# Performance work log

Measured on AMD Instinct MI355X. Metric: run time of the kernel, lower is better.

The kernel has to match this reference:

```python
import jax, jax.numpy as jnp
import numpy as np

K = 64
N = 1000000
J = 100000
B = 1048576


def setup_inputs() -> dict:
    key = jax.random.key(0)
    k1, k2, k3, k4, k5, k6, k7 = jax.random.split(key, 7)
    users = jax.random.randint(k1, (B,), 0, N, dtype=jnp.int64) if jax.config.jax_enable_x64 else jax.random.randint(k1, (B,), 0, N, dtype=jnp.int32)
    jokes = jax.random.randint(k2, (B,), 0, J, dtype=jnp.int64) if jax.config.jax_enable_x64 else jax.random.randint(k2, (B,), 0, J, dtype=jnp.int32)
    U = jax.random.normal(k3, (N, K), dtype=jnp.float32)
    V = jax.random.normal(k4, (J, K), dtype=jnp.float32)
    a = jax.random.normal(k5, (N, 1), dtype=jnp.float32)
    b = jax.random.normal(k6, (J, 1), dtype=jnp.float32)
    g = jax.random.normal(k7, (1,), dtype=jnp.float32)
    return {"users": users, "jokes": jokes, "U": U, "V": V, "a": a, "b": b, "g": g}


def reference(users, jokes, U, V, a, b, g):
    # gather latent factors and biases, fused dot + bias adds
    u = U[users]              # [B, K]
    v = V[jokes]              # [B, K]
    dot = jnp.sum(u * v, axis=-1)          # per-row dot product (bmm equivalent)
    r = dot + a[users, 0] + b[jokes, 0] + g  # broadcasts g:[1] -> [B]
    return r
```

## Files before the change

### kernel.cpp

```cpp
#include <hip/hip_runtime.h>


constexpr int KV  = 16;
constexpr int RPG = 4;

__global__ __launch_bounds__(256) void latent_linear_kernel(
    const int* __restrict__ users,
    const int* __restrict__ jokes,
    const float* __restrict__ U,
    const float* __restrict__ V,
    const float* __restrict__ a,
    const float* __restrict__ b,
    const float* __restrict__ g,
    float* __restrict__ out,
    int B)
{
    const int sub        = threadIdx.x & 15;
    const int grp_local  = threadIdx.x >> 4;
    const int grps_per_b = blockDim.x >> 4;
    const int grp_stride = gridDim.x * grps_per_b;
    const int ngroups    = B / RPG;

    const float4* __restrict__ U4 = reinterpret_cast<const float4*>(U);
    const float4* __restrict__ V4 = reinterpret_cast<const float4*>(V);
    const int4*   __restrict__ users4 = reinterpret_cast<const int4*>(users);
    const int4*   __restrict__ jokes4 = reinterpret_cast<const int4*>(jokes);

    const float g0 = g[0];

    int grp = blockIdx.x * grps_per_b + grp_local;

    if (blockIdx.x == 0 && threadIdx.x == 0) {
        for (int row = ngroups * RPG; row < B; ++row) {
            const int ui = users[row], ji = jokes[row];
            float d = 0.f;
            for (int k = 0; k < 64; ++k) d += U[(size_t)ui * 64 + k] * V[(size_t)ji * 64 + k];
            out[row] = d + a[ui] + b[ji] + g0;
        }
    }

    if (grp >= ngroups) return;

    int4 u4 = users4[grp];
    int4 j4 = jokes4[grp];

    while (grp < ngroups) {
        const int ui[RPG] = {u4.x, u4.y, u4.z, u4.w};
        const int ji[RPG] = {j4.x, j4.y, j4.z, j4.w};

        float4 uu[RPG], vv[RPG];
#pragma unroll
        for (int r = 0; r < RPG; ++r) {
            uu[r] = U4[(size_t)ui[r] * KV + sub];
            vv[r] = V4[(size_t)ji[r] * KV + sub];
        }

        float ab[RPG], bb[RPG];
#pragma unroll
        for (int r = 0; r < RPG; ++r) {
            ab[r] = a[ui[r]];
            bb[r] = b[ji[r]];
        }

        const int next = grp + grp_stride;
        if (next < ngroups) {
            u4 = users4[next];
            j4 = jokes4[next];
        }

        const int base = grp * RPG;
#pragma unroll
        for (int r = 0; r < RPG; ++r) {
            float d = uu[r].x * vv[r].x + uu[r].y * vv[r].y
                    + uu[r].z * vv[r].z + uu[r].w * vv[r].w;
            d += __shfl_down(d, 8, 16);
            d += __shfl_down(d, 4, 16);
            d += __shfl_down(d, 2, 16);
            d += __shfl_down(d, 1, 16);
            if (sub == 0)
                out[base + r] = d + ab[r] + bb[r] + g0;
        }

        grp = next;
    }
}

extern "C" void kernel_launch(void* const* d_in, const int* in_sizes, int n_in,
                              void* d_out, int out_size, void* d_ws, size_t ws_size,
                              hipStream_t stream)
{
    const int*   users = (const int*)d_in[0];
    const int*   jokes = (const int*)d_in[1];
    const float* U     = (const float*)d_in[2];
    const float* V     = (const float*)d_in[3];
    const float* a     = (const float*)d_in[4];
    const float* b     = (const float*)d_in[5];
    const float* g     = (const float*)d_in[6];
    float*       out   = (float*)d_out;

    const int B = in_sizes[0];

    const int block = 256;
    int grid = 2048;
    const int ngroups = B / RPG;
    const int max_grid = (ngroups + (block / 16) - 1) / (block / 16);
    if (grid > max_grid) grid = max_grid > 0 ? max_grid : 1;

    latent_linear_kernel<<<grid, block, 0, stream>>>(users, jokes, U, V, a, b, g, out, B);
}
```

Measured before the change: 387.3 us.

## Bucket-sort rows by user index before gathering latent factors

Adds a histogram, scan and scatter pass that bucket-sorts the batch rows by user id into 4096 buckets. The compute kernel then walks the sorted order, so U-row gathers become roughly monotone and more cache/DRAM-page friendly, and it scatters results back to the original row positions. In exchange it adds four extra kernel launches, atomics on the global cursors, and extra traffic for sortedUi/sortedRow. The jokes and out accesses also become random.

```diff
diff --git a/kernel.cpp b/kernel.cpp
--- a/kernel.cpp
+++ b/kernel.cpp
@@ -3,9 +3,63 @@
 
 constexpr int KV  = 16;
 constexpr int RPG = 4;
+constexpr int NB  = 4096;
 
-__global__ __launch_bounds__(256) void latent_linear_kernel(
-    const int* __restrict__ users,
+__global__ __launch_bounds__(256) void zero_kernel(unsigned* __restrict__ counts) {
+    int i = blockIdx.x * blockDim.x + threadIdx.x;
+    if (i < NB) counts[i] = 0u;
+}
+
+__global__ __launch_bounds__(256) void hist_kernel(const int* __restrict__ users,
+                                                   unsigned* __restrict__ counts,
+                                                   int B, int shift) {
+    __shared__ unsigned h[NB];
+    for (int j = threadIdx.x; j < NB; j += 256) h[j] = 0u;
+    __syncthreads();
+    for (int i = blockIdx.x * blockDim.x + threadIdx.x; i < B; i += gridDim.x * blockDim.x)
+        atomicAdd(&h[((unsigned)users[i]) >> shift], 1u);
+    __syncthreads();
+    for (int j = threadIdx.x; j < NB; j += 256) {
+        unsigned c = h[j];
+        if (c) atomicAdd(&counts[j], c);
+    }
+}
+
+__global__ __launch_bounds__(256) void scan_kernel(const unsigned* __restrict__ counts,
+                                                   unsigned* __restrict__ cursor) {
+    __shared__ unsigned psum[256];
+    const int t = threadIdx.x;
+    unsigned local[16];
+    unsigned s = 0;
+    for (int k = 0; k < 16; ++k) { local[k] = counts[t * 16 + k]; s += local[k]; }
+    psum[t] = s;
+    __syncthreads();
+    for (int off = 1; off < 256; off <<= 1) {
+        unsigned v = (t >= off) ? psum[t - off] : 0u;
+        __syncthreads();
+        psum[t] += v;
+        __syncthreads();
+    }
+    unsigned base = (t == 0) ? 0u : psum[t - 1];
+    for (int k = 0; k < 16; ++k) { cursor[t * 16 + k] = base; base += local[k]; }
+}
+
+__global__ __launch_bounds__(256) void scatter_kernel(const int* __restrict__ users,
+                                                      unsigned* __restrict__ cursor,
+                                                      unsigned* __restrict__ sortedUi,
+                                                      unsigned* __restrict__ sortedRow,
+                                                      int B, int shift) {
+    for (int i = blockIdx.x * blockDim.x + threadIdx.x; i < B; i += gridDim.x * blockDim.x) {
+        const unsigned ui = (unsigned)users[i];
+        const unsigned pos = atomicAdd(&cursor[ui >> shift], 1u);
+        sortedUi[pos]  = ui;
+        sortedRow[pos] = (unsigned)i;
+    }
+}
+
+__global__ __launch_bounds__(256) void compute_kernel(
+    const unsigned* __restrict__ sortedUi,
+    const unsigned* __restrict__ sortedRow,
     const int* __restrict__ jokes,
     const float* __restrict__ U,
     const float* __restrict__ V,
@@ -15,38 +69,23 @@
     float* __restrict__ out,
     int B)
 {
-    const int sub        = threadIdx.x & 15;
-    const int grp_local  = threadIdx.x >> 4;
-    const int grps_per_b = blockDim.x >> 4;
-    const int grp_stride = gridDim.x * grps_per_b;
-    const int ngroups    = B / RPG;
+    const int sub = threadIdx.x & 15;
+    const int grp = blockIdx.x * 16 + (threadIdx.x >> 4);
+    const int ng  = B / RPG;
 
     const float4* __restrict__ U4 = reinterpret_cast<const float4*>(U);
     const float4* __restrict__ V4 = reinterpret_cast<const float4*>(V);
-    const int4*   __restrict__ users4 = reinterpret_cast<const int4*>(users);
-    const int4*   __restrict__ jokes4 = reinterpret_cast<const int4*>(jokes);
-
     const float g0 = g[0];
 
-    int grp = blockIdx.x * grps_per_b + grp_local;
+    if (grp < ng) {
+        const uint4 su = reinterpret_cast<const uint4*>(sortedUi)[grp];
+        const uint4 sr = reinterpret_cast<const uint4*>(sortedRow)[grp];
+        const unsigned ui[RPG]   = {su.x, su.y, su.z, su.w};
+        const unsigned orig[RPG] = {sr.x, sr.y, sr.z, sr.w};
 
-    if (blockIdx.x == 0 && threadIdx.x == 0) {
-        for (int row = ngroups * RPG; row < B; ++row) {
-            const int ui = users[row], ji = jokes[row];
-            float d = 0.f;
-            for (int k = 0; k < 64; ++k) d += U[(size_t)ui * 64 + k] * V[(size_t)ji * 64 + k];
-            out[row] = d + a[ui] + b[ji] + g0;
-        }
-    }
-
-    if (grp >= ngroups) return;
-
-    int4 u4 = users4[grp];
-    int4 j4 = jokes4[grp];
-
-    while (grp < ngroups) {
-        const int ui[RPG] = {u4.x, u4.y, u4.z, u4.w};
-        const int ji[RPG] = {j4.x, j4.y, j4.z, j4.w};
+        int ji[RPG];
+#pragma unroll
+        for (int r = 0; r < RPG; ++r) ji[r] = jokes[orig[r]];
 
         float4 uu[RPG], vv[RPG];
 #pragma unroll
@@ -57,18 +96,8 @@
 
         float ab[RPG], bb[RPG];
 #pragma unroll
-        for (int r = 0; r < RPG; ++r) {
-            ab[r] = a[ui[r]];
-            bb[r] = b[ji[r]];
-        }
+        for (int r = 0; r < RPG; ++r) { ab[r] = a[ui[r]]; bb[r] = b[ji[r]]; }
 
-        const int next = grp + grp_stride;
-        if (next < ngroups) {
-            u4 = users4[next];
-            j4 = jokes4[next];
-        }
-
-        const int base = grp * RPG;
 #pragma unroll
         for (int r = 0; r < RPG; ++r) {
             float d = uu[r].x * vv[r].x + uu[r].y * vv[r].y
@@ -78,10 +107,19 @@
             d += __shfl_down(d, 2, 16);
             d += __shfl_down(d, 1, 16);
             if (sub == 0)
-                out[base + r] = d + ab[r] + bb[r] + g0;
+                out[orig[r]] = d + ab[r] + bb[r] + g0;
         }
+    }
 
-        grp = next;
+    if (blockIdx.x == 0 && threadIdx.x == 0) {
+        for (int p = ng * RPG; p < B; ++p) {
+            const unsigned ui = sortedUi[p];
+            const unsigned orig = sortedRow[p];
+            const int ji = jokes[orig];
+            float d = 0.f;
+            for (int k = 0; k < 64; ++k) d += U[(size_t)ui * 64 + k] * V[(size_t)ji * 64 + k];
+            out[orig] = d + a[ui] + b[ji] + g0;
+        }
     }
 }
 
@@ -99,12 +137,23 @@
     float*       out   = (float*)d_out;
 
     const int B = in_sizes[0];
+    const int N = in_sizes[2] / 64;
 
-    const int block = 256;
-    int grid = 2048;
-    const int ngroups = B / RPG;
-    const int max_grid = (ngroups + (block / 16) - 1) / (block / 16);
-    if (grid > max_grid) grid = max_grid > 0 ? max_grid : 1;
+    int shift = 0;
+    while ((((long long)(N - 1)) >> shift) >= NB) ++shift;
 
-    latent_linear_kernel<<<grid, block, 0, stream>>>(users, jokes, U, V, a, b, g, out, B);
+    unsigned* wsu       = (unsigned*)d_ws;
+    unsigned* counts    = wsu;
+    unsigned* cursor    = wsu + NB;
+    unsigned* sortedUi  = wsu + 2 * NB;
+    unsigned* sortedRow = sortedUi + B;
+
+    zero_kernel<<<(NB + 255) / 256, 256, 0, stream>>>(counts);
+    hist_kernel<<<128, 256, 0, stream>>>(users, counts, B, shift);
+    scan_kernel<<<1, 256, 0, stream>>>(counts, cursor);
+    scatter_kernel<<<512, 256, 0, stream>>>(users, cursor, sortedUi, sortedRow, B, shift);
+
+    const int ng = B / RPG;
+    const int grid = (ng + 15) / 16;
+    compute_kernel<<<grid, 256, 0, stream>>>(sortedUi, sortedRow, jokes, U, V, a, b, g, out, B);
 }
```

Result: slower. 487.3 us (+25.8%).
